# Kernel optimization log

Hardware: AMD Instinct MI355X
Metric: run time of the kernel (lower is better)

## Reference

```python
import jax, jax.numpy as jnp
import numpy as np

TOP_K = 8
NUM_EXPERTS = 128
HIDDEN = 2048
TOKENS = 16384
NORM_TOPK_PROB = True


def setup_inputs() -> dict:
    key = jax.random.key(0)
    k1, k2 = jax.random.split(key)
    hidden_states = jax.random.normal(k1, (TOKENS, HIDDEN), dtype=jnp.float32)
    # gate weight [num_experts, hidden] (nn.Linear layout)
    weight = jax.random.normal(k2, (NUM_EXPERTS, HIDDEN), dtype=jnp.float32) * 0.02
    return {"hidden_states": hidden_states, "weight": weight}


def reference(hidden_states, weight):
    x = hidden_states.reshape(-1, HIDDEN)
    # router_logits: [tokens, num_experts]
    router_logits = jnp.einsum("td,ed->te", x, weight)
    router_probs = jax.nn.softmax(router_logits.astype(jnp.float32), axis=-1)
    top_vals, top_idx = jax.lax.top_k(router_probs, TOP_K)
    if NORM_TOPK_PROB:
        top_vals = top_vals / jnp.sum(top_vals, axis=-1, keepdims=True)
    top_vals = top_vals.astype(hidden_states.dtype)
    return router_logits, top_vals, top_idx
```

## Files before the change

### kernel.cpp

```cpp
#include <hip/hip_runtime.h>
#include <float.h>
#include <math.h>

#define TOKENS 16384
#define HIDDEN 2048
#define NEXP 128
#define TOPK 8
#define NCAND 12
#define DELTA 5e-4f

#define BM 32
#define KSTEPS (HIDDEN / 16)

typedef float f32x16 __attribute__((ext_vector_type(16)));
typedef short bf16x8 __attribute__((ext_vector_type(8)));

__device__ __forceinline__ unsigned pack_hi(float a, float b) {
    return (__float_as_uint(a) >> 16) | (__float_as_uint(b) & 0xFFFF0000u);
}
__device__ __forceinline__ float resid(float a) {
    return a - __uint_as_float(__float_as_uint(a) & 0xFFFF0000u);
}

__device__ __forceinline__ bf16x8 pack8_hi(const float4 a, const float4 b) {
    union { uint4 u; bf16x8 v; } t;
    t.u.x = pack_hi(a.x, a.y); t.u.y = pack_hi(a.z, a.w);
    t.u.z = pack_hi(b.x, b.y); t.u.w = pack_hi(b.z, b.w);
    return t.v;
}
__device__ __forceinline__ bf16x8 pack8_lo(const float4 a, const float4 b) {
    union { uint4 u; bf16x8 v; } t;
    t.u.x = pack_hi(resid(a.x), resid(a.y)); t.u.y = pack_hi(resid(a.z), resid(a.w));
    t.u.z = pack_hi(resid(b.x), resid(b.y)); t.u.w = pack_hi(resid(b.z), resid(b.w));
    return t.v;
}

__global__ __launch_bounds__(256) void presplit_w(const float* __restrict__ W,
                                                  unsigned short* __restrict__ Ws) {
    const int c = blockIdx.x * 256 + threadIdx.x;
    const int lane = c & 63;
    const int q = c >> 6;
    const int hl = q & 1;
    const int nt = (q >> 1) & 3;
    const int k16 = q >> 3;
    const int e = nt * 32 + (lane & 31);
    const int k0 = k16 * 16 + (lane >> 5) * 8;
    const float* wp = W + (size_t)e * HIDDEN + k0;
    float4 a = *(const float4*)wp;
    float4 b = *(const float4*)(wp + 4);
    if (hl) {
        a.x = resid(a.x); a.y = resid(a.y); a.z = resid(a.z); a.w = resid(a.w);
        b.x = resid(b.x); b.y = resid(b.y); b.z = resid(b.z); b.w = resid(b.w);
    }
    uint4 o;
    o.x = pack_hi(a.x, a.y); o.y = pack_hi(a.z, a.w);
    o.z = pack_hi(b.x, b.y); o.w = pack_hi(b.z, b.w);
    *(uint4*)(Ws + (size_t)c * 8) = o;
}

__global__ __launch_bounds__(256) void router_gemm(const float* __restrict__ X,
                                                   const unsigned short* __restrict__ Ws,
                                                   float* __restrict__ logits) {
    const int tid = threadIdx.x;
    const int lane = tid & 63;
    const int wid = tid >> 6;
    const int t0 = blockIdx.x * BM;

    const float* xp = X + (size_t)(t0 + (lane & 31)) * HIDDEN + (lane >> 5) * 8;
    const unsigned short* bp = Ws + (size_t)(wid * 2) * 512 + (size_t)lane * 8;

    f32x16 acc;
#pragma unroll
    for (int r = 0; r < 16; ++r) acc[r] = 0.f;

    float4 xa[4], xb[4];
    bf16x8 bh[4], bl[4];
#pragma unroll
    for (int i = 0; i < 4; ++i) {
        xa[i] = *(const float4*)(xp + i * 16);
        xb[i] = *(const float4*)(xp + i * 16 + 4);
        bh[i] = *(const bf16x8*)(bp + (size_t)i * 4096);
        bl[i] = *(const bf16x8*)(bp + (size_t)i * 4096 + 512);
    }

#pragma unroll 1
    for (int kt = 0; kt < KSTEPS; kt += 4) {
#pragma unroll
        for (int i = 0; i < 4; ++i) {
            const bf16x8 ah = pack8_hi(xa[i], xb[i]);
            const bf16x8 al = pack8_lo(xa[i], xb[i]);
            acc = __builtin_amdgcn_mfma_f32_32x32x16_bf16(ah, bh[i], acc, 0, 0, 0);
            acc = __builtin_amdgcn_mfma_f32_32x32x16_bf16(ah, bl[i], acc, 0, 0, 0);
            acc = __builtin_amdgcn_mfma_f32_32x32x16_bf16(al, bh[i], acc, 0, 0, 0);
            int kn = kt + 4 + i; if (kn > KSTEPS - 1) kn = KSTEPS - 1;
            xa[i] = *(const float4*)(xp + kn * 16);
            xb[i] = *(const float4*)(xp + kn * 16 + 4);
            bh[i] = *(const bf16x8*)(bp + (size_t)kn * 4096);
            bl[i] = *(const bf16x8*)(bp + (size_t)kn * 4096 + 512);
        }
        __builtin_amdgcn_s_barrier();
    }

    const int e = wid * 32 + (lane & 31);
    const int rbase = 4 * (lane >> 5);
#pragma unroll
    for (int reg = 0; reg < 16; ++reg) {
        const int row = (reg & 3) + 8 * (reg >> 2) + rbase;
        logits[(size_t)(t0 + row) * NEXP + e] = acc[reg];
    }
}

__global__ __launch_bounds__(256) void router_topk(const float* __restrict__ logits,
                                                   const float* __restrict__ X,
                                                   const float* __restrict__ W,
                                                   float* __restrict__ top_vals,
                                                   float* __restrict__ top_idx) {
    const int lane = threadIdx.x & 63;
    const int t = blockIdx.x * 4 + (threadIdx.x >> 6);
    const float* lrow = logits + (size_t)t * NEXP;
    const float l0 = lrow[lane];
    const float l1 = lrow[lane + 64];
    bool r0 = false, r1 = false;
    float vals[NCAND]; int idxs[NCAND];

#pragma unroll
    for (int it = 0; it < TOPK + 1; ++it) {
        const float c0 = r0 ? -FLT_MAX : l0;
        const float c1 = r1 ? -FLT_MAX : l1;
        float v; int id;
        if (c1 > c0) { v = c1; id = lane + 64; }
        else         { v = c0; id = lane; }
#pragma unroll
        for (int off = 1; off < 64; off <<= 1) {
            const float ov = __shfl_xor(v, off);
            const int   oi = __shfl_xor(id, off);
            if (ov > v || (ov == v && oi < id)) { v = ov; id = oi; }
        }
        vals[it] = v; idxs[it] = id;
        if (id == lane) r0 = true;
        else if (id == lane + 64) r1 = true;
    }

    float ming = FLT_MAX;
#pragma unroll
    for (int i = 0; i < TOPK; ++i) ming = fminf(ming, vals[i] - vals[i + 1]);

    if (ming >= DELTA) {
        if (lane == 0) {
            const float m = vals[0];
            float ex[TOPK], s = 0.f;
#pragma unroll
            for (int i = 0; i < TOPK; ++i) { ex[i] = expf(vals[i] - m); s += ex[i]; }
            const float inv = 1.f / s;
#pragma unroll
            for (int i = 0; i < TOPK; ++i) {
                top_vals[(size_t)t * TOPK + i] = ex[i] * inv;
                top_idx[(size_t)t * TOPK + i] = (float)idxs[i];
            }
        }
        return;
    }

#pragma unroll
    for (int it = TOPK + 1; it < NCAND; ++it) {
        const float c0 = r0 ? -FLT_MAX : l0;
        const float c1 = r1 ? -FLT_MAX : l1;
        float v; int id;
        if (c1 > c0) { v = c1; id = lane + 64; }
        else         { v = c0; id = lane; }
#pragma unroll
        for (int off = 1; off < 64; off <<= 1) {
            const float ov = __shfl_xor(v, off);
            const int   oi = __shfl_xor(id, off);
            if (ov > v || (ov == v && oi < id)) { v = ov; id = oi; }
        }
        vals[it] = v; idxs[it] = id;
        if (id == lane) r0 = true;
        else if (id == lane + 64) r1 = true;
    }

    const float* xr = X + (size_t)t * HIDDEN;
    double xd[32];
#pragma unroll
    for (int j = 0; j < 8; ++j) {
        const float4 v = *(const float4*)(xr + j * 256 + lane * 4);
        xd[j * 4 + 0] = (double)v.x; xd[j * 4 + 1] = (double)v.y;
        xd[j * 4 + 2] = (double)v.z; xd[j * 4 + 3] = (double)v.w;
    }
    double acc[NCAND];
#pragma unroll
    for (int c = 0; c < NCAND; ++c) {
        const float* wr = W + (size_t)idxs[c] * HIDDEN;
        double a0 = 0.0, a1 = 0.0;
#pragma unroll
        for (int j = 0; j < 8; ++j) {
            const float4 w = *(const float4*)(wr + j * 256 + lane * 4);
            a0 = fma((double)w.x, xd[j * 4 + 0], a0);
            a1 = fma((double)w.y, xd[j * 4 + 1], a1);
            a0 = fma((double)w.z, xd[j * 4 + 2], a0);
            a1 = fma((double)w.w, xd[j * 4 + 3], a1);
        }
        acc[c] = a0 + a1;
    }
#pragma unroll
    for (int c = 0; c < NCAND; ++c)
#pragma unroll
        for (int off = 1; off < 64; off <<= 1)
            acc[c] += __shfl_xor(acc[c], off);

    int rank[NCAND];
#pragma unroll
    for (int c = 0; c < NCAND; ++c) {
        int r = 0;
#pragma unroll
        for (int m = 0; m < NCAND; ++m)
            if (acc[m] > acc[c] || (acc[m] == acc[c] && idxs[m] < idxs[c])) ++r;
        rank[c] = r;
    }
    double vmax = acc[0];
#pragma unroll
    for (int c = 0; c < NCAND; ++c) if (rank[c] == 0) vmax = acc[c];
    float ex[NCAND], s = 0.f;
#pragma unroll
    for (int c = 0; c < NCAND; ++c) {
        ex[c] = (rank[c] < TOPK) ? expf((float)(acc[c] - vmax)) : 0.f;
        s += ex[c];
    }
    const float inv = 1.f / s;
    if (lane == 0) {
#pragma unroll
        for (int c = 0; c < NCAND; ++c)
            if (rank[c] < TOPK) {
                top_vals[(size_t)t * TOPK + rank[c]] = ex[c] * inv;
                top_idx[(size_t)t * TOPK + rank[c]] = (float)idxs[c];
            }
    }
}

extern "C" void kernel_launch(void* const* d_in, const int* in_sizes, int n_in,
                              void* d_out, int out_size, void* d_ws, size_t ws_size,
                              hipStream_t stream) {
    const float* X = (const float*)d_in[0];
    const float* W = (const float*)d_in[1];
    float* logits = (float*)d_out;
    float* tvals  = logits + (size_t)TOKENS * NEXP;
    float* tidx   = tvals + (size_t)TOKENS * TOPK;

    unsigned short* Wsplit = (unsigned short*)d_ws;

    presplit_w<<<256, 256, 0, stream>>>(W, Wsplit);
    router_gemm<<<TOKENS / BM, 256, 0, stream>>>(X, Wsplit, logits);
    router_topk<<<TOKENS / 4, 256, 0, stream>>>(logits, X, W, tvals, tidx);
}
```

Measured before the change: 308.3 us.

## Stage router GEMM tiles through double-buffered LDS with direct global-to-LDS loads

The router GEMM now copies X and the pre-split weight tiles straight into double-buffered shared memory using global_load_lds, with an XOR swizzle on the X tile. Each wave reads its MFMA fragments from LDS instead of holding per-lane register prefetches. This is meant to hide global memory latency behind the MFMA work and to coalesce the loads. In exchange it adds LDS traffic, two barriers per K step and a larger shared-memory footprint, which is why launch bounds now request two blocks per CU.

```diff
diff --git a/kernel.cpp b/kernel.cpp
--- a/kernel.cpp
+++ b/kernel.cpp
@@ -10,7 +10,8 @@
 #define DELTA 5e-4f
 
 #define BM 32
-#define KSTEPS (HIDDEN / 16)
+#define BK 64
+#define KIT (HIDDEN / BK)
 
 typedef float f32x16 __attribute__((ext_vector_type(16)));
 typedef short bf16x8 __attribute__((ext_vector_type(8)));
@@ -33,6 +34,12 @@
     t.u.x = pack_hi(resid(a.x), resid(a.y)); t.u.y = pack_hi(resid(a.z), resid(a.w));
     t.u.z = pack_hi(resid(b.x), resid(b.y)); t.u.w = pack_hi(resid(b.z), resid(b.w));
     return t.v;
+}
+
+__device__ __forceinline__ void load_lds_16B(const void* g, void* l) {
+    __builtin_amdgcn_global_load_lds(
+        (const __attribute__((address_space(1))) unsigned int*)g,
+        (__attribute__((address_space(3))) unsigned int*)l, 16, 0, 0);
 }
 
 __global__ __launch_bounds__(256) void presplit_w(const float* __restrict__ W,
@@ -58,48 +65,87 @@
     *(uint4*)(Ws + (size_t)c * 8) = o;
 }
 
-__global__ __launch_bounds__(256) void router_gemm(const float* __restrict__ X,
-                                                   const unsigned short* __restrict__ Ws,
-                                                   float* __restrict__ logits) {
+__global__ __launch_bounds__(256, 2) void router_gemm(const float* __restrict__ X,
+                                                      const unsigned short* __restrict__ Ws,
+                                                      float* __restrict__ logits) {
+    __shared__ float sA[2][BM * BK];
+    __shared__ unsigned short sB[2][32 * 512];
+
     const int tid = threadIdx.x;
     const int lane = tid & 63;
     const int wid = tid >> 6;
     const int t0 = blockIdx.x * BM;
 
-    const float* xp = X + (size_t)(t0 + (lane & 31)) * HIDDEN + (lane >> 5) * 8;
-    const unsigned short* bp = Ws + (size_t)(wid * 2) * 512 + (size_t)lane * 8;
+    const int ai0 = wid * 2, ai1 = wid * 2 + 1;
+    const int ar0 = 4 * ai0 + (lane >> 4);
+    const int ar1 = 4 * ai1 + (lane >> 4);
+    const int ak0 = ((lane & 15) ^ (ar0 & 15)) * 4;
+    const int ak1 = ((lane & 15) ^ (ar1 & 15)) * 4;
+    const float* aSrc0 = X + (size_t)(t0 + ar0) * HIDDEN + ak0;
+    const float* aSrc1 = X + (size_t)(t0 + ar1) * HIDDEN + ak1;
+    const unsigned short* bSrc = Ws + ((size_t)wid * 8) * 512 + (size_t)lane * 8;
+
+    const int cr = lane & 31;
+    const int kb = (lane >> 5) * 2;
+    int aoff[4][2];
+#pragma unroll
+    for (int s = 0; s < 4; ++s) {
+        aoff[s][0] = cr * 64 + (((s * 4 + kb + 0) ^ (cr & 15)) * 4);
+        aoff[s][1] = cr * 64 + (((s * 4 + kb + 1) ^ (cr & 15)) * 4);
+    }
+    const int boff = (wid * 2) * 512 + lane * 8;
 
     f32x16 acc;
 #pragma unroll
     for (int r = 0; r < 16; ++r) acc[r] = 0.f;
 
-    float4 xa[4], xb[4];
-    bf16x8 bh[4], bl[4];
-#pragma unroll
-    for (int i = 0; i < 4; ++i) {
-        xa[i] = *(const float4*)(xp + i * 16);
-        xb[i] = *(const float4*)(xp + i * 16 + 4);
-        bh[i] = *(const bf16x8*)(bp + (size_t)i * 4096);
-        bl[i] = *(const bf16x8*)(bp + (size_t)i * 4096 + 512);
-    }
+#pragma unroll
+    for (int kt = 0; kt < 2; ++kt) {
+        load_lds_16B(aSrc0 + kt * BK, &sA[kt][ai0 * 256]);
+        load_lds_16B(aSrc1 + kt * BK, &sA[kt][ai1 * 256]);
+#pragma unroll
+        for (int i = 0; i < 8; ++i)
+            load_lds_16B(bSrc + ((size_t)kt * 32 + i) * 512, &sB[kt][(wid * 8 + i) * 512]);
+    }
+    asm volatile("s_waitcnt vmcnt(10)" ::: "memory");
+    __builtin_amdgcn_s_barrier();
+    asm volatile("" ::: "memory");
 
 #pragma unroll 1
-    for (int kt = 0; kt < KSTEPS; kt += 4) {
-#pragma unroll
-        for (int i = 0; i < 4; ++i) {
-            const bf16x8 ah = pack8_hi(xa[i], xb[i]);
-            const bf16x8 al = pack8_lo(xa[i], xb[i]);
-            acc = __builtin_amdgcn_mfma_f32_32x32x16_bf16(ah, bh[i], acc, 0, 0, 0);
-            acc = __builtin_amdgcn_mfma_f32_32x32x16_bf16(ah, bl[i], acc, 0, 0, 0);
-            acc = __builtin_amdgcn_mfma_f32_32x32x16_bf16(al, bh[i], acc, 0, 0, 0);
-            int kn = kt + 4 + i; if (kn > KSTEPS - 1) kn = KSTEPS - 1;
-            xa[i] = *(const float4*)(xp + kn * 16);
-            xb[i] = *(const float4*)(xp + kn * 16 + 4);
-            bh[i] = *(const bf16x8*)(bp + (size_t)kn * 4096);
-            bl[i] = *(const bf16x8*)(bp + (size_t)kn * 4096 + 512);
-        }
+    for (int kt = 0; kt < KIT; ++kt) {
+        const int cur = kt & 1;
+        const float* aBuf = &sA[cur][0];
+        const unsigned short* bBuf = &sB[cur][0];
+
+#pragma unroll
+        for (int s = 0; s < 4; ++s) {
+            const float4 f0 = *(const float4*)(aBuf + aoff[s][0]);
+            const float4 f1 = *(const float4*)(aBuf + aoff[s][1]);
+            const bf16x8 ah = pack8_hi(f0, f1);
+            const bf16x8 al = pack8_lo(f0, f1);
+            const bf16x8 bh = *(const bf16x8*)(bBuf + boff + s * 4096);
+            const bf16x8 bl = *(const bf16x8*)(bBuf + boff + s * 4096 + 512);
+            acc = __builtin_amdgcn_mfma_f32_32x32x16_bf16(ah, bh, acc, 0, 0, 0);
+            acc = __builtin_amdgcn_mfma_f32_32x32x16_bf16(ah, bl, acc, 0, 0, 0);
+            acc = __builtin_amdgcn_mfma_f32_32x32x16_bf16(al, bh, acc, 0, 0, 0);
+        }
+
         __builtin_amdgcn_s_barrier();
-    }
+        asm volatile("" ::: "memory");
+
+        int kn = kt + 2; if (kn > KIT - 1) kn = KIT - 1;
+        load_lds_16B(aSrc0 + kn * BK, &sA[cur][ai0 * 256]);
+        load_lds_16B(aSrc1 + kn * BK, &sA[cur][ai1 * 256]);
+#pragma unroll
+        for (int i = 0; i < 8; ++i)
+            load_lds_16B(bSrc + ((size_t)kn * 32 + i) * 512, &sB[cur][(wid * 8 + i) * 512]);
+
+        asm volatile("s_waitcnt vmcnt(10)" ::: "memory");
+        __builtin_amdgcn_sched_barrier(0);
+        __builtin_amdgcn_s_barrier();
+        asm volatile("" ::: "memory");
+    }
+    asm volatile("s_waitcnt vmcnt(0)" ::: "memory");
 
     const int e = wid * 32 + (lane & 31);
     const int rbase = 4 * (lane >> 5);
```

Measured after the change: 276.7 us. 10.3% less time.
